# Performance work log

Hardware: AMD Instinct MI355X
Metric: run time of the kernel (lower is better)

Reference implementation:

```python
import jax, jax.numpy as jnp
import numpy as np

N_NODES = 50000
N_EDGES = 800000
HID = 128


def setup_inputs() -> dict:
    key = jax.random.key(0)
    ks = jax.random.split(key, 10)
    s_msg = 1.0 / np.sqrt(2 * HID + 1)
    s_u1 = 1.0 / np.sqrt(2 * HID)
    s_u2 = 1.0 / np.sqrt(HID)
    return {
        "z": jax.random.normal(ks[0], (N_NODES, HID), dtype=jnp.float32),
        "edge_weight": jax.random.uniform(ks[1], (N_EDGES,), dtype=jnp.float32),
        "edge_src": jax.random.randint(ks[2], (N_EDGES,), 0, N_NODES),
        "edge_dst": jax.random.randint(ks[3], (N_EDGES,), 0, N_NODES),
        "Wm": jax.random.normal(ks[4], (2 * HID + 1, HID), dtype=jnp.float32) * s_msg,
        "bm": jax.random.normal(ks[5], (HID,), dtype=jnp.float32) * s_msg,
        "W1": jax.random.normal(ks[6], (2 * HID, HID), dtype=jnp.float32) * s_u1,
        "b1": jax.random.normal(ks[7], (HID,), dtype=jnp.float32) * s_u1,
        "W2": jax.random.normal(ks[8], (HID, HID), dtype=jnp.float32) * s_u2,
        "b2": jax.random.normal(ks[9], (HID,), dtype=jnp.float32) * s_u2,
    }


def reference(z, edge_weight, edge_src, edge_dst, Wm, bm, W1, b1, W2, b2):
    n, H = z.shape
    # message Linear on concat([z[u], z[v], w]) split to avoid materializing [E, 2H+1]
    Wd, Ws, ww = Wm[:H], Wm[H:2 * H], Wm[2 * H]  # [H,H], [H,H], [H]
    msgs = (z[edge_dst] @ Wd + z[edge_src] @ Ws
            + edge_weight[:, None] * ww[None, :] + bm)  # [E, H]
    # max-aggregate messages per destination node; zeros for isolated nodes
    agg = jax.ops.segment_max(msgs, edge_dst, num_segments=n)  # [n, H], -inf if empty
    deg = jax.ops.segment_sum(jnp.ones_like(edge_weight), edge_dst, num_segments=n)
    agg = jnp.where(deg[:, None] > 0, agg, jnp.zeros((), dtype=z.dtype))
    # update MLP on concat([z, agg]) split into two GEMMs
    W1a, W1b = W1[:H], W1[H:]
    hidden = jax.nn.relu(z @ W1a + agg @ W1b + b1)  # [n, H]
    return hidden @ W2 + b2  # [n, H]
```

## Files before the change

### kernel.cpp

```cpp
#include <hip/hip_runtime.h>
#include <hip/hip_bf16.h>

#define HID 128

typedef short bf16x8 __attribute__((ext_vector_type(8)));
typedef float f32x4  __attribute__((ext_vector_type(4)));
typedef unsigned short u16;
typedef unsigned long long u64;

__device__ __forceinline__ u16 f2bf(float f) {
    __hip_bfloat16 h = __float2bfloat16(f);
    return *reinterpret_cast<u16*>(&h);
}
__device__ __forceinline__ float bf2f(u16 x) {
    unsigned u = ((unsigned)x) << 16;
    return __uint_as_float(u);
}
__device__ __forceinline__ u64 pack_rec(int dst, int src, float w) {
    int wq = (int)fmaf(w, 32768.f, 0.5f);
    wq = wq > 32767 ? 32767 : wq;
    return ((u64)(unsigned)dst << 31) | ((unsigned)src << 15) | (unsigned)wq;
}


__global__ __launch_bounds__(256)
void prep_hist(const float* __restrict__ z, const float* __restrict__ Wm,
               const float* __restrict__ W1, const float* __restrict__ W2,
               const int* __restrict__ edst,
               u16* __restrict__ Ab, u16* __restrict__ Wt, int* __restrict__ bhist,
               int N, int Mp, int E, int bz, int bw, int nbk)
{
    __shared__ int lh[256];
    const int b = blockIdx.x;
    const int t = threadIdx.x;
    if (b < bz) {
        const int idx4 = (b * 256 + t) * 4;
        if (idx4 >= Mp * 128) return;
        const int row = idx4 >> 7, col = idx4 & 127;
        ushort4 u;
        if (row < N) {
            const float4 v = *(const float4*)&z[(size_t)row * 128 + col];
            u.x = f2bf(v.x); u.y = f2bf(v.y); u.z = f2bf(v.z); u.w = f2bf(v.w);
        } else { u.x = 0; u.y = 0; u.z = 0; u.w = 0; }
        *(ushort4*)&Ab[(size_t)row * 256 + col] = u;
    } else if (b < bz + bw) {
        const int idx = (b - bz) * 256 + t;
        if (idx >= 81920) return;
        float v;
        if (idx < 32768) {
            const int nn = idx >> 7, k = idx & 127;
            v = (nn < 128) ? Wm[k * 128 + nn] : Wm[(128 + k) * 128 + (nn - 128)];
        } else if (idx < 65536) {
            const int j = idx - 32768, n = j >> 8, k = j & 255;
            v = W1[k * 128 + n];
        } else {
            const int j = idx - 65536, n = j >> 7, k = j & 127;
            v = W2[k * 128 + n];
        }
        Wt[idx] = f2bf(v);
    } else {
        lh[t] = 0;
        __syncthreads();
        const int e0 = (b - bz - bw) * 4096;
        const int eend = min(e0 + 4096, E);
        for (int e = e0 + t; e < eend; e += 256)
            atomicAdd(&lh[edst[e] >> 8], 1);
        __syncthreads();
        if (t < nbk && lh[t] > 0) atomicAdd(&bhist[t], lh[t]);
    }
}

__global__ __launch_bounds__(256)
void scatter_gemmP(const int* __restrict__ esrc, const int* __restrict__ edst,
                   const float* __restrict__ ew,
                   const int* __restrict__ bhist, int* __restrict__ brun,
                   u64* __restrict__ tmp, int E, int nbk, int nsc,
                   const u16* __restrict__ Ab, const u16* __restrict__ Wds_t,
                   u16* __restrict__ Pb, int Mp)
{
    __shared__ int cnt[256];
    __shared__ int rbase[256];
    __shared__ int bbase[256];
    __shared__ u16 As[64 * 136];
    const int t = threadIdx.x;

    if (blockIdx.x < nsc) {
        const int e0 = blockIdx.x * 4096;
        const int eend = min(e0 + 4096, E);

        cnt[t] = 0;
        if (t == 0) {
            int run = 0;
            for (int i = 0; i < nbk; i++) { bbase[i] = run; run += bhist[i]; }
        }
        __syncthreads();

        if (eend - e0 == 4096) {
            int myb[16]; u64 myrec[16];
#pragma unroll
            for (int i = 0; i < 16; i++) {
                const int e = e0 + t + i * 256;
                const int d = edst[e];
                myb[i] = d >> 8;
                myrec[i] = pack_rec(d, esrc[e], ew[e]);
                atomicAdd(&cnt[myb[i]], 1);
            }
            __syncthreads();
            if (t < nbk && cnt[t] > 0) rbase[t] = bbase[t] + atomicAdd(&brun[t], cnt[t]);
            __syncthreads();
            cnt[t] = 0;
            __syncthreads();
#pragma unroll
            for (int i = 0; i < 16; i++) {
                const int r = atomicAdd(&cnt[myb[i]], 1);
                tmp[(size_t)rbase[myb[i]] + r] = myrec[i];
            }
        } else {
            for (int e = e0 + t; e < eend; e += 256)
                atomicAdd(&cnt[edst[e] >> 8], 1);
            __syncthreads();
            if (t < nbk && cnt[t] > 0) rbase[t] = bbase[t] + atomicAdd(&brun[t], cnt[t]);
            __syncthreads();
            cnt[t] = 0;
            __syncthreads();
            for (int e = e0 + t; e < eend; e += 256) {
                const int d = edst[e];
                const int bk = d >> 8;
                const int r = atomicAdd(&cnt[bk], 1);
                tmp[(size_t)rbase[bk] + r] = pack_rec(d, esrc[e], ew[e]);
            }
        }
    } else {
        const int row0 = (blockIdx.x - nsc) * 64;
        const int wv = t >> 6, lane = t & 63;
        const int wy = wv & 1, wx = wv >> 1;
        const int q = lane >> 4, n = lane & 15;

#pragma unroll
        for (int i = 0; i < 4; i++) {
            const int chunk = i * 256 + t;
            const int row = chunk >> 4;
            const int c8 = chunk & 15;
            *(bf16x8*)&As[row * 136 + c8 * 8] =
                *(const bf16x8*)&Ab[(size_t)(row0 + row) * 256 + c8 * 8];
        }
        __syncthreads();

        const u16* pAl = As + (wy * 32 + n) * 136 + q * 8;
        const u16* pB = Wds_t + (size_t)(wx * 128 + n) * 128 + q * 8;

        f32x4 acc[2][8];
#pragma unroll
        for (int i = 0; i < 2; i++)
#pragma unroll
            for (int j = 0; j < 8; j++) acc[i][j] = f32x4{0.f, 0.f, 0.f, 0.f};

#pragma unroll
        for (int kk = 0; kk < 128; kk += 32) {
            bf16x8 a0 = *(const bf16x8*)(pAl + kk);
            bf16x8 a1 = *(const bf16x8*)(pAl + 16 * 136 + kk);
            bf16x8 bfr[8];
#pragma unroll
            for (int ni = 0; ni < 8; ni++)
                bfr[ni] = *(const bf16x8*)(pB + (size_t)ni * 16 * 128 + kk);
#pragma unroll
            for (int ni = 0; ni < 8; ni++) {
                acc[0][ni] = __builtin_amdgcn_mfma_f32_16x16x32_bf16(a0, bfr[ni], acc[0][ni], 0, 0, 0);
                acc[1][ni] = __builtin_amdgcn_mfma_f32_16x16x32_bf16(a1, bfr[ni], acc[1][ni], 0, 0, 0);
            }
        }

#pragma unroll
        for (int mi = 0; mi < 2; mi++) {
#pragma unroll
            for (int ni = 0; ni < 8; ni++) {
                const int rbase2 = row0 + wy * 32 + mi * 16 + q * 4;
                const int c = wx * 128 + ni * 16 + n;
#pragma unroll
                for (int r = 0; r < 4; r++)
                    Pb[(size_t)(rbase2 + r) * 256 + c] = f2bf(acc[mi][ni][r]);
            }
        }
    }
}

__global__ __launch_bounds__(256)
void bucket_sort(const u64* __restrict__ tmp, const int* __restrict__ bhist,
                 int* __restrict__ offsets, unsigned* __restrict__ s_ew,
                 int N, int E, int nbk)
{
    __shared__ int cnt[256];
    __shared__ int cur[256];
    __shared__ int ps[256];
    __shared__ int sh_base[2];
    const int b = blockIdx.x;
    const int t = threadIdx.x;
    const int n0 = b << 8;
    const int nhi = min(256, N - n0);

    if (t == 0) {
        int run = 0;
        for (int i = 0; i < b; i++) run += bhist[i];
        sh_base[0] = run;
        sh_base[1] = run + bhist[b];
    }
    cnt[t] = 0;
    __syncthreads();
    const int base = sh_base[0];
    const int endp = sh_base[1];

    for (int r = base + t; r < endp; r += 256)
        atomicAdd(&cnt[(int)(tmp[r] >> 31) - n0], 1);
    __syncthreads();

    const int v = cnt[t];
    ps[t] = v;
    __syncthreads();
    for (int off = 1; off < 256; off <<= 1) {
        int add = (t >= off) ? ps[t - off] : 0;
        __syncthreads();
        ps[t] += add;
        __syncthreads();
    }
    cur[t] = base + ps[t] - v;
    __syncthreads();

    if (t < nhi) offsets[n0 + t] = cur[t];
    if (t == 0 && n0 + nhi == N) offsets[N] = E;

    for (int r = base + t; r < endp; r += 256) {
        const u64 rec = tmp[r];
        const int local = (int)(rec >> 31) - n0;
        const int pos = atomicAdd(&cur[local], 1);
        s_ew[pos] = (unsigned)(rec & 0x7FFFFFFFu);
    }
}

__global__ __launch_bounds__(256)
void aggregate_kernel(const u16* __restrict__ Pb,
                      const float* __restrict__ bm,
                      const float* __restrict__ ww,
                      const int* __restrict__ offsets,
                      const unsigned* __restrict__ s_ew,
                      u16* __restrict__ Ab, int N, int Mp)
{
    const int t = threadIdx.x;
    const int lane = t & 63;
    const int nd = blockIdx.x * 4 + (t >> 6);
    if (nd >= Mp) return;
    const int h0 = lane * 2;
    u16* dst = &Ab[(size_t)nd * 256 + 128 + h0];
    if (nd >= N) { *(ushort2*)dst = make_ushort2(0, 0); return; }

    const int start = offsets[nd];
    const int end   = offsets[nd + 1];
    const float ww0 = ww[h0], ww1 = ww[h0 + 1];
    const float kq = 1.f / 32768.f;
    float m0 = -INFINITY, m1 = -INFINITY;

    int e = start;
    for (; e + 7 < end; e += 8) {
        unsigned u[8]; ushort2 zz[8];
#pragma unroll
        for (int i = 0; i < 8; i++) u[i] = s_ew[e + i];
#pragma unroll
        for (int i = 0; i < 8; i++)
            zz[i] = *(const ushort2*)&Pb[(size_t)(u[i] >> 15) * 256 + 128 + h0];
        float ma[8], mb[8];
#pragma unroll
        for (int i = 0; i < 8; i++) {
            const float wq = (float)(u[i] & 32767u) * kq;
            ma[i] = fmaf(wq, ww0, bf2f(zz[i].x));
            mb[i] = fmaf(wq, ww1, bf2f(zz[i].y));
        }
        m0 = fmaxf(m0, fmaxf(fmaxf(fmaxf(ma[0], ma[1]), fmaxf(ma[2], ma[3])),
                             fmaxf(fmaxf(ma[4], ma[5]), fmaxf(ma[6], ma[7]))));
        m1 = fmaxf(m1, fmaxf(fmaxf(fmaxf(mb[0], mb[1]), fmaxf(mb[2], mb[3])),
                             fmaxf(fmaxf(mb[4], mb[5]), fmaxf(mb[6], mb[7]))));
    }
    for (; e < end; e++) {
        const unsigned u0 = s_ew[e];
        const float w0 = (float)(u0 & 32767u) * kq;
        const ushort2 z0 = *(const ushort2*)&Pb[(size_t)(u0 >> 15) * 256 + 128 + h0];
        m0 = fmaxf(m0, fmaf(w0, ww0, bf2f(z0.x)));
        m1 = fmaxf(m1, fmaf(w0, ww1, bf2f(z0.y)));
    }

    ushort2 outv;
    if (end > start) {
        const ushort2 zd = *(const ushort2*)&Pb[(size_t)nd * 256 + h0];
        outv.x = f2bf(bf2f(zd.x) + bm[h0]     + m0);
        outv.y = f2bf(bf2f(zd.y) + bm[h0 + 1] + m1);
    } else { outv.x = 0; outv.y = 0; }
    *(ushort2*)dst = outv;
}

__global__ __launch_bounds__(256)
void gemm_HO(const u16* __restrict__ Ab, const u16* __restrict__ W1t,
             const float* __restrict__ b1, const u16* __restrict__ W2t,
             const float* __restrict__ b2, float* __restrict__ out, int Mstore)
{
    __shared__ u16 smem[64 * 264];

    const int row0 = blockIdx.x * 64;
    const int tid = threadIdx.x;
    const int wv = tid >> 6, lane = tid & 63;
    const int wy = wv & 1, wx = wv >> 1;
    const int q = lane >> 4, n = lane & 15;

#pragma unroll
    for (int i = 0; i < 8; i++) {
        const int chunk = i * 256 + tid;
        const int row = chunk >> 5;
        const int c8 = chunk & 31;
        *(bf16x8*)&smem[row * 264 + c8 * 8] =
            *(const bf16x8*)&Ab[(size_t)(row0 + row) * 256 + c8 * 8];
    }
    __syncthreads();

    f32x4 acc[2][4];

    {
        const u16* pAl = smem + (wy * 32 + n) * 264 + q * 8;
        const u16* pB = W1t + (size_t)(wx * 64 + n) * 256 + q * 8;

#pragma unroll
        for (int i = 0; i < 2; i++)
#pragma unroll
            for (int j = 0; j < 4; j++) acc[i][j] = f32x4{0.f, 0.f, 0.f, 0.f};

#pragma unroll
        for (int kk = 0; kk < 256; kk += 32) {
            bf16x8 b0 = *(const bf16x8*)(pB + kk);
            bf16x8 b1f = *(const bf16x8*)(pB + 16 * 256 + kk);
            bf16x8 b2f = *(const bf16x8*)(pB + 32 * 256 + kk);
            bf16x8 b3f = *(const bf16x8*)(pB + 48 * 256 + kk);
            bf16x8 a0 = *(const bf16x8*)(pAl + kk);
            bf16x8 a1 = *(const bf16x8*)(pAl + 16 * 264 + kk);
            acc[0][0] = __builtin_amdgcn_mfma_f32_16x16x32_bf16(a0, b0,  acc[0][0], 0, 0, 0);
            acc[0][1] = __builtin_amdgcn_mfma_f32_16x16x32_bf16(a0, b1f, acc[0][1], 0, 0, 0);
            acc[0][2] = __builtin_amdgcn_mfma_f32_16x16x32_bf16(a0, b2f, acc[0][2], 0, 0, 0);
            acc[0][3] = __builtin_amdgcn_mfma_f32_16x16x32_bf16(a0, b3f, acc[0][3], 0, 0, 0);
            acc[1][0] = __builtin_amdgcn_mfma_f32_16x16x32_bf16(a1, b0,  acc[1][0], 0, 0, 0);
            acc[1][1] = __builtin_amdgcn_mfma_f32_16x16x32_bf16(a1, b1f, acc[1][1], 0, 0, 0);
            acc[1][2] = __builtin_amdgcn_mfma_f32_16x16x32_bf16(a1, b2f, acc[1][2], 0, 0, 0);
            acc[1][3] = __builtin_amdgcn_mfma_f32_16x16x32_bf16(a1, b3f, acc[1][3], 0, 0, 0);
        }
    }
    __syncthreads();

#pragma unroll
    for (int mi = 0; mi < 2; mi++) {
#pragma unroll
        for (int ni = 0; ni < 4; ni++) {
            const int rl = wy * 32 + mi * 16 + q * 4;
            const int c = wx * 64 + ni * 16 + n;
#pragma unroll
            for (int r = 0; r < 4; r++) {
                float v = acc[mi][ni][r] + b1[c];
                smem[(rl + r) * 136 + c] = f2bf(fmaxf(v, 0.f));
            }
        }
    }
    __syncthreads();

    {
        const u16* pB = W2t + (size_t)(wx * 64 + n) * 128 + q * 8;
        const u16* pHl = smem + (wy * 32 + n) * 136 + q * 8;

#pragma unroll
        for (int i = 0; i < 2; i++)
#pragma unroll
            for (int j = 0; j < 4; j++) acc[i][j] = f32x4{0.f, 0.f, 0.f, 0.f};

#pragma unroll
        for (int kk = 0; kk < 128; kk += 32) {
            bf16x8 b0 = *(const bf16x8*)(pB + kk);
            bf16x8 b1f = *(const bf16x8*)(pB + 16 * 128 + kk);
            bf16x8 b2f = *(const bf16x8*)(pB + 32 * 128 + kk);
            bf16x8 b3f = *(const bf16x8*)(pB + 48 * 128 + kk);
            bf16x8 a0 = *(const bf16x8*)(pHl + kk);
            bf16x8 a1 = *(const bf16x8*)(pHl + 16 * 136 + kk);
            acc[0][0] = __builtin_amdgcn_mfma_f32_16x16x32_bf16(a0, b0,  acc[0][0], 0, 0, 0);
            acc[0][1] = __builtin_amdgcn_mfma_f32_16x16x32_bf16(a0, b1f, acc[0][1], 0, 0, 0);
            acc[0][2] = __builtin_amdgcn_mfma_f32_16x16x32_bf16(a0, b2f, acc[0][2], 0, 0, 0);
            acc[0][3] = __builtin_amdgcn_mfma_f32_16x16x32_bf16(a0, b3f, acc[0][3], 0, 0, 0);
            acc[1][0] = __builtin_amdgcn_mfma_f32_16x16x32_bf16(a1, b0,  acc[1][0], 0, 0, 0);
            acc[1][1] = __builtin_amdgcn_mfma_f32_16x16x32_bf16(a1, b1f, acc[1][1], 0, 0, 0);
            acc[1][2] = __builtin_amdgcn_mfma_f32_16x16x32_bf16(a1, b2f, acc[1][2], 0, 0, 0);
            acc[1][3] = __builtin_amdgcn_mfma_f32_16x16x32_bf16(a1, b3f, acc[1][3], 0, 0, 0);
        }

#pragma unroll
        for (int mi = 0; mi < 2; mi++) {
#pragma unroll
            for (int ni = 0; ni < 4; ni++) {
                const int rbase = row0 + wy * 32 + mi * 16 + q * 4;
                const int c = wx * 64 + ni * 16 + n;
#pragma unroll
                for (int r = 0; r < 4; r++) {
                    const int rr = rbase + r;
                    if (rr >= Mstore) continue;
                    out[(size_t)rr * 128 + c] = acc[mi][ni][r] + b2[c];
                }
            }
        }
    }
}

extern "C" void kernel_launch(void* const* d_in, const int* in_sizes, int n_in,
                              void* d_out, int out_size, void* d_ws, size_t ws_size,
                              hipStream_t stream) {
    const float* z    = (const float*)d_in[0];
    const float* ew   = (const float*)d_in[1];
    const int*   esrc = (const int*)d_in[2];
    const int*   edst = (const int*)d_in[3];
    const float* Wm   = (const float*)d_in[4];
    const float* bm   = (const float*)d_in[5];
    const float* W1   = (const float*)d_in[6];
    const float* b1   = (const float*)d_in[7];
    const float* W2   = (const float*)d_in[8];
    const float* b2   = (const float*)d_in[9];
    float* out = (float*)d_out;

    const int N  = in_sizes[0] / HID;
    const int E  = in_sizes[1];
    const int Mp = ((N + 63) / 64) * 64;
    const int nbk = (N + 255) / 256;

    char* w = (char*)d_ws;
    u16*  Ab      = (u16*)w;      w += (size_t)Mp * 256 * 2;
    u16*  Pb      = (u16*)w;      w += (size_t)Mp * 256 * 2;
    u16*  Wt      = (u16*)w;      w += (size_t)81920 * 2;
    int*  offsets = (int*)w;      w += (size_t)(N + 64) * 4;
    int*  bhist   = (int*)w;      w += 256 * 4;
    int*  brun    = (int*)w;      w += 256 * 4;
    unsigned* s_ew = (unsigned*)w; w += (size_t)E * 4;
    u64*  tmp     = (u64*)w;      w += (size_t)E * 8;

    const int bz = (Mp * 32 + 255) / 256;
    const int bw = (81920 + 255) / 256;
    const int bh = (E + 4095) / 4096;
    const int nsc = (E + 4095) / 4096;

    hipMemsetAsync(bhist, 0, 512 * sizeof(int), stream);
    prep_hist<<<bz + bw + bh, 256, 0, stream>>>(z, Wm, W1, W2, edst, Ab, Wt, bhist,
                                                N, Mp, E, bz, bw, nbk);
    scatter_gemmP<<<nsc + Mp / 64, 256, 0, stream>>>(esrc, edst, ew, bhist, brun,
                                                     tmp, E, nbk, nsc,
                                                     Ab, Wt, Pb, Mp);
    bucket_sort<<<nbk, 256, 0, stream>>>(tmp, bhist, offsets, s_ew, N, E, nbk);
    aggregate_kernel<<<(Mp + 3) / 4, 256, 0, stream>>>(Pb, bm, Wm + 256 * 128,
                                                       offsets, s_ew, Ab, N, Mp);
    gemm_HO<<<Mp / 64, 256, 0, stream>>>(Ab, Wt + 32768, b1, Wt + 65536, b2, out, N);
}
```

Measured before the change: 218.1 us.

## Split aggregate wavefront into four edge groups with 16-byte row gathers

The max-aggregation kernel changes its thread mapping. Each lane now owns 8 contiguous hidden channels and loads them with one 16-byte gather, so a 16-lane group covers a full 256-byte row. The four groups in a wavefront handle different edges in parallel, and their partial maxima are combined with cross-lane shuffles. This gives wider, fewer memory transactions and more edges in flight per wave. In exchange it adds clamped redundant loads when degree is not a multiple of 8, plus a shuffle reduction per node.

```diff
diff --git a/kernel.cpp b/kernel.cpp
--- a/kernel.cpp
+++ b/kernel.cpp
@@ -246,53 +246,72 @@
 {
     const int t = threadIdx.x;
     const int lane = t & 63;
+    const int g = lane >> 4;
+    const int c0 = (lane & 15) * 8;
     const int nd = blockIdx.x * 4 + (t >> 6);
     if (nd >= Mp) return;
-    const int h0 = lane * 2;
-    u16* dst = &Ab[(size_t)nd * 256 + 128 + h0];
-    if (nd >= N) { *(ushort2*)dst = make_ushort2(0, 0); return; }
-
-    const int start = offsets[nd];
-    const int end   = offsets[nd + 1];
-    const float ww0 = ww[h0], ww1 = ww[h0 + 1];
+
+    u16* dst = &Ab[(size_t)nd * 256 + 128 + c0];
+
+    int start = 0, end = 0;
+    if (nd < N) { start = offsets[nd]; end = offsets[nd + 1]; }
+
+    if (end <= start) {
+        if (g == 0) {
+            bf16x8 zv = {0, 0, 0, 0, 0, 0, 0, 0};
+            *(bf16x8*)dst = zv;
+        }
+        return;
+    }
+
+    float wwv[8];
+    {
+        const float4 wa = *(const float4*)&ww[c0];
+        const float4 wb = *(const float4*)&ww[c0 + 4];
+        wwv[0] = wa.x; wwv[1] = wa.y; wwv[2] = wa.z; wwv[3] = wa.w;
+        wwv[4] = wb.x; wwv[5] = wb.y; wwv[6] = wb.z; wwv[7] = wb.w;
+    }
+
     const float kq = 1.f / 32768.f;
-    float m0 = -INFINITY, m1 = -INFINITY;
-
-    int e = start;
-    for (; e + 7 < end; e += 8) {
-        unsigned u[8]; ushort2 zz[8];
-#pragma unroll
-        for (int i = 0; i < 8; i++) u[i] = s_ew[e + i];
-#pragma unroll
-        for (int i = 0; i < 8; i++)
-            zz[i] = *(const ushort2*)&Pb[(size_t)(u[i] >> 15) * 256 + 128 + h0];
-        float ma[8], mb[8];
-#pragma unroll
-        for (int i = 0; i < 8; i++) {
-            const float wq = (float)(u[i] & 32767u) * kq;
-            ma[i] = fmaf(wq, ww0, bf2f(zz[i].x));
-            mb[i] = fmaf(wq, ww1, bf2f(zz[i].y));
-        }
-        m0 = fmaxf(m0, fmaxf(fmaxf(fmaxf(ma[0], ma[1]), fmaxf(ma[2], ma[3])),
-                             fmaxf(fmaxf(ma[4], ma[5]), fmaxf(ma[6], ma[7]))));
-        m1 = fmaxf(m1, fmaxf(fmaxf(fmaxf(mb[0], mb[1]), fmaxf(mb[2], mb[3])),
-                             fmaxf(fmaxf(mb[4], mb[5]), fmaxf(mb[6], mb[7]))));
-    }
-    for (; e < end; e++) {
-        const unsigned u0 = s_ew[e];
-        const float w0 = (float)(u0 & 32767u) * kq;
-        const ushort2 z0 = *(const ushort2*)&Pb[(size_t)(u0 >> 15) * 256 + 128 + h0];
-        m0 = fmaxf(m0, fmaf(w0, ww0, bf2f(z0.x)));
-        m1 = fmaxf(m1, fmaf(w0, ww1, bf2f(z0.y)));
-    }
-
-    ushort2 outv;
-    if (end > start) {
-        const ushort2 zd = *(const ushort2*)&Pb[(size_t)nd * 256 + h0];
-        outv.x = f2bf(bf2f(zd.x) + bm[h0]     + m0);
-        outv.y = f2bf(bf2f(zd.y) + bm[h0 + 1] + m1);
-    } else { outv.x = 0; outv.y = 0; }
-    *(ushort2*)dst = outv;
+    float m[8];
+#pragma unroll
+    for (int j = 0; j < 8; j++) m[j] = -INFINITY;
+
+    const int last = end - 1;
+    for (int eb = start; eb < end; eb += 8) {
+        int ea = eb + g;      if (ea > last) ea = last;
+        int ec = eb + 4 + g;  if (ec > last) ec = last;
+        const unsigned u0 = s_ew[ea];
+        const unsigned u1 = s_ew[ec];
+        const bf16x8 p0 = *(const bf16x8*)&Pb[(size_t)(u0 >> 15) * 256 + 128 + c0];
+        const bf16x8 p1 = *(const bf16x8*)&Pb[(size_t)(u1 >> 15) * 256 + 128 + c0];
+        const float wA = (float)(u0 & 32767u) * kq;
+        const float wB = (float)(u1 & 32767u) * kq;
+#pragma unroll
+        for (int j = 0; j < 8; j++)
+            m[j] = fmaxf(m[j], fmaf(wA, wwv[j], bf2f((u16)p0[j])));
+#pragma unroll
+        for (int j = 0; j < 8; j++)
+            m[j] = fmaxf(m[j], fmaf(wB, wwv[j], bf2f((u16)p1[j])));
+    }
+
+#pragma unroll
+    for (int j = 0; j < 8; j++) {
+        m[j] = fmaxf(m[j], __shfl_xor(m[j], 16));
+        m[j] = fmaxf(m[j], __shfl_xor(m[j], 32));
+    }
+
+    if (g == 0) {
+        const bf16x8 zd = *(const bf16x8*)&Pb[(size_t)nd * 256 + c0];
+        const float4 ba = *(const float4*)&bm[c0];
+        const float4 bb = *(const float4*)&bm[c0 + 4];
+        const float bmv[8] = {ba.x, ba.y, ba.z, ba.w, bb.x, bb.y, bb.z, bb.w};
+        bf16x8 outv;
+#pragma unroll
+        for (int j = 0; j < 8; j++)
+            outv[j] = (short)f2bf(bf2f((u16)zd[j]) + bmv[j] + m[j]);
+        *(bf16x8*)dst = outv;
+    }
 }
 
 __global__ __launch_bounds__(256)
```

After: 210.0 us. 3.7% less time.
